# Kernel tuning notes

Measured on AMD Instinct MI355X. Metric: run time of the kernel, lower is better.

Reference implementation:

```python
import jax, jax.numpy as jnp
import numpy as np

DX = 0.5
N_STEPS = 8


def _bilinear_sample(vf, p):
    """Batched bilinear interpolation of vf at points p, clipping to the image domain.
    vf: (B, 2, H, W). p: (B, 2, H, W) with p[:,0]=x (along W), p[:,1]=y (along H)."""
    B, C, H, W = vf.shape
    x = jnp.clip(p[:, 0], 0.0, W - 1.0)
    y = jnp.clip(p[:, 1], 0.0, H - 1.0)
    x0 = jnp.floor(x)
    y0 = jnp.floor(y)
    x1 = jnp.minimum(x0 + 1.0, W - 1.0)
    y1 = jnp.minimum(y0 + 1.0, H - 1.0)
    wx = (x - x0)[:, None]  # (B,1,H,W)
    wy = (y - y0)[:, None]
    x0i, x1i = x0.astype(jnp.int32), x1.astype(jnp.int32)
    y0i, y1i = y0.astype(jnp.int32), y1.astype(jnp.int32)
    vf_flat = vf.reshape(B, C, H * W)

    def gather(yi, xi):
        idx = (yi * W + xi).reshape(B, 1, H * W)
        return jnp.take_along_axis(vf_flat, idx, axis=2).reshape(B, C, H, W)

    v00 = gather(y0i, x0i)
    v01 = gather(y0i, x1i)
    v10 = gather(y1i, x0i)
    v11 = gather(y1i, x1i)
    return (v00 * (1.0 - wx) * (1.0 - wy) + v01 * wx * (1.0 - wy)
            + v10 * (1.0 - wx) * wy + v11 * wx * wy)


def _init_values(B, H, W, dtype):
    # torch: stack(meshgrid(arange(H), arange(W), indexing='ij')[::-1]) -> channel0=x, channel1=y
    gx, gy = jnp.meshgrid(jnp.arange(W, dtype=dtype), jnp.arange(H, dtype=dtype))  # (H,W)
    return jnp.broadcast_to(jnp.stack([gx, gy], axis=0)[None], (B, 2, H, W))


def _trajectories(vf, dx=DX, n_steps=N_STEPS):
    """Euler IVP integration of every pixel through vf. Returns (n_steps+1, B, 2, H, W)."""
    B, C, H, W = vf.shape
    init = _init_values(B, H, W, vf.dtype)

    def step(p, _):
        p_next = p + dx * _bilinear_sample(vf, p)  # euler step
        return p_next, p_next

    _, traj = jax.lax.scan(step, init, None, length=n_steps)
    return jnp.concatenate([init[None], traj], axis=0)


def setup_inputs() -> dict:
    key = jax.random.key(0)
    k1, k2 = jax.random.split(key)
    B, H, W = 8, 512, 512
    vf_pred = jax.random.normal(k1, (B, 2, H, W), dtype=jnp.float32)
    vf_true = jax.random.normal(k2, (B, 2, H, W), dtype=jnp.float32)
    return {"vf_pred": vf_pred, "vf_true": vf_true}


def reference(vf_pred, vf_true):
    true_traj = _trajectories(vf_true)
    pred_traj = _trajectories(vf_pred)
    return jnp.mean((true_traj - pred_traj) ** 2)
```

## Files before the change

kernel.cpp:

```cpp
#include <hip/hip_runtime.h>
#include <hip/hip_fp16.h>

#define HH 512
#define WW 512
#define BB 8
#define HW (HH * WW)
#define DXS 0.5f
#define NSTEPS 8

#define R_BLK 4
#define BAND 15
#define LSW 520

typedef float f2  __attribute__((ext_vector_type(2)));
typedef float f4a __attribute__((ext_vector_type(4)));
typedef unsigned int u4a __attribute__((ext_vector_type(4)));

__device__ __forceinline__ f2 h2f(unsigned int h) {
    __half2 v = __builtin_bit_cast(__half2, h);
    float2 f = __half22float2(v);
    return (f2){f.x, f.y};
}
__device__ __forceinline__ unsigned int f2h(float a, float b) {
    __half2 h = __floats2half2_rn(a, b);
    return __builtin_bit_cast(unsigned int, h);
}

__device__ __forceinline__ f2 bilin_lds(const unsigned int* __restrict__ lds,
                                        int band_lo,
                                        const float* __restrict__ g0,
                                        const float* __restrict__ g1,
                                        float px, float py) {
    float x = fminf(fmaxf(px, 0.0f), (float)(WW - 1));
    float y = fminf(fmaxf(py, 0.0f), (float)(HH - 1));
    float x0f = fminf(floorf(x), (float)(WW - 2));
    float y0f = fminf(floorf(y), (float)(HH - 2));
    float wx = x - x0f;
    float wy = y - y0f;
    int xi = (int)x0f;
    int yi = (int)y0f;
    int r = yi - band_lo;
    f2 out;
    if (r >= 0 && r <= BAND - 2) {
        int idx = r * LSW + xi;
        unsigned int a0 = lds[idx];
        unsigned int a1 = lds[idx + 1];
        unsigned int b0 = lds[idx + LSW];
        unsigned int b1 = lds[idx + LSW + 1];
        f2 v00 = h2f(a0), v01 = h2f(a1), v10 = h2f(b0), v11 = h2f(b1);
        f2 top = v00 + wx * (v01 - v00);
        f2 bot = v10 + wx * (v11 - v10);
        out = top + wy * (bot - top);
    } else {
        int i00 = yi * WW + xi;
        float w00 = (1.0f - wx) * (1.0f - wy);
        float w01 = wx * (1.0f - wy);
        float w10 = (1.0f - wx) * wy;
        float w11 = wx * wy;
        out.x = g0[i00] * w00 + g0[i00 + 1] * w01 + g0[i00 + WW] * w10 + g0[i00 + WW + 1] * w11;
        out.y = g1[i00] * w00 + g1[i00 + 1] * w01 + g1[i00 + WW] * w10 + g1[i00 + WW + 1] * w11;
    }
    return out;
}

__global__ __launch_bounds__(256) void ivp_loss_lds(const float* __restrict__ vf_pred,
                                                    const float* __restrict__ vf_true,
                                                    double* __restrict__ acc) {
    __shared__ unsigned int lt[BAND * LSW];
    __shared__ unsigned int lp[BAND * LSW];
    __shared__ float wsum[4];

    int b    = blockIdx.x & 7;
    int rb   = blockIdx.x >> 3;
    int base = rb * R_BLK;
    int band_lo = min(max(base - 5, 0), HH - BAND);

    const float* tg0 = vf_true + (size_t)b * 2 * HW;
    const float* tg1 = tg0 + HW;
    const float* pg0 = vf_pred + (size_t)b * 2 * HW;
    const float* pg1 = pg0 + HW;

    for (int i = threadIdx.x; i < BAND * 128; i += 256) {
        int rl = i >> 7;
        int g  = i & 127;
        int off = (band_lo + rl) * WW + g * 4;
        f4a tx = *(const f4a*)(tg0 + off);
        f4a ty = *(const f4a*)(tg1 + off);
        f4a px = *(const f4a*)(pg0 + off);
        f4a py = *(const f4a*)(pg1 + off);
        u4a wt = { f2h(tx.x, ty.x), f2h(tx.y, ty.y), f2h(tx.z, ty.z), f2h(tx.w, ty.w) };
        u4a wp = { f2h(px.x, py.x), f2h(px.y, py.y), f2h(px.z, py.z), f2h(px.w, py.w) };
        *(u4a*)&lt[rl * LSW + g * 4] = wt;
        *(u4a*)&lp[rl * LSW + g * 4] = wp;
    }
    __syncthreads();

    int lane = threadIdx.x & 63;
    int wv   = threadIdx.x >> 6;
    int row  = base + wv;
    float fy = (float)row;

    float ptx[8], pty[8], ppx[8], ppy[8];
    float sum = 0.0f;

    #pragma unroll
    for (int c = 0; c < 8; ++c) {
        int x  = lane + 64 * c;
        int li = (row - band_lo) * LSW + x;
        f2 vt = h2f(lt[li]);
        f2 vp = h2f(lp[li]);
        float fx = (float)x;
        ptx[c] = fmaf(DXS, vt.x, fx);  pty[c] = fmaf(DXS, vt.y, fy);
        ppx[c] = fmaf(DXS, vp.x, fx);  ppy[c] = fmaf(DXS, vp.y, fy);
        float dx = ptx[c] - ppx[c], dy = pty[c] - ppy[c];
        sum += dx * dx + dy * dy;
    }

    #pragma unroll 1
    for (int s = 1; s < NSTEPS; ++s) {
        #pragma unroll
        for (int c = 0; c < 8; ++c) {
            f2 vt = bilin_lds(lt, band_lo, tg0, tg1, ptx[c], pty[c]);
            f2 vp = bilin_lds(lp, band_lo, pg0, pg1, ppx[c], ppy[c]);
            ptx[c] += DXS * vt.x;  pty[c] += DXS * vt.y;
            ppx[c] += DXS * vp.x;  ppy[c] += DXS * vp.y;
            float dx = ptx[c] - ppx[c], dy = pty[c] - ppy[c];
            sum += dx * dx + dy * dy;
        }
    }

    for (int off = 32; off > 0; off >>= 1)
        sum += __shfl_down(sum, off, 64);
    if (lane == 0) wsum[wv] = sum;
    __syncthreads();
    if (threadIdx.x == 0) {
        double blocksum = (double)wsum[0] + (double)wsum[1]
                        + (double)wsum[2] + (double)wsum[3];
        atomicAdd(acc, blocksum);
    }
}

__global__ void ivp_finalize_kernel(const double* __restrict__ acc,
                                    float* __restrict__ out) {
    const double total = (double)(NSTEPS + 1) * BB * 2 * HW;
    out[0] = (float)(acc[0] / total);
}

extern "C" void kernel_launch(void* const* d_in, const int* in_sizes, int n_in,
                              void* d_out, int out_size, void* d_ws, size_t ws_size,
                              hipStream_t stream) {
    const float* vf_pred = (const float*)d_in[0];
    const float* vf_true = (const float*)d_in[1];
    float* out = (float*)d_out;
    double* acc = (double*)d_ws;

    hipMemsetAsync(d_ws, 0, 16, stream);

    int blocks = BB * (HH / R_BLK);
    ivp_loss_lds<<<blocks, 256, 0, stream>>>(vf_pred, vf_true, acc);
    ivp_finalize_kernel<<<1, 1, 0, stream>>>(acc, out);
}
```

Before: 56.00 us.

## Fuse finalize into main kernel, use half2 bilinear math, shrink LDS stride

Removes the separate finalize kernel launch by having the last block, found through an atomic counter, compute the mean. The LDS bilinear path now interpolates in packed half2 FMA instead of converting each corner to float. The LDS row stride drops from 520 to 512 so the index can be a shift, at the risk of more bank conflicts. Doing the interpolation in half precision adds rounding error to the trajectories.

```diff
diff --git a/kernel.cpp b/kernel.cpp
--- a/kernel.cpp
+++ b/kernel.cpp
@@ -10,7 +10,7 @@
 
 #define R_BLK 4
 #define BAND 15
-#define LSW 520
+#define LSW 512
 
 typedef float f2  __attribute__((ext_vector_type(2)));
 typedef float f4a __attribute__((ext_vector_type(4)));
@@ -41,16 +41,19 @@
     int yi = (int)y0f;
     int r = yi - band_lo;
     f2 out;
-    if (r >= 0 && r <= BAND - 2) {
-        int idx = r * LSW + xi;
-        unsigned int a0 = lds[idx];
-        unsigned int a1 = lds[idx + 1];
-        unsigned int b0 = lds[idx + LSW];
-        unsigned int b1 = lds[idx + LSW + 1];
-        f2 v00 = h2f(a0), v01 = h2f(a1), v10 = h2f(b0), v11 = h2f(b1);
-        f2 top = v00 + wx * (v01 - v00);
-        f2 bot = v10 + wx * (v11 - v10);
-        out = top + wy * (bot - top);
+    if ((unsigned)r <= (unsigned)(BAND - 2)) {
+        int idx = (r << 9) + xi;
+        __half2 v00 = __builtin_bit_cast(__half2, lds[idx]);
+        __half2 v01 = __builtin_bit_cast(__half2, lds[idx + 1]);
+        __half2 v10 = __builtin_bit_cast(__half2, lds[idx + LSW]);
+        __half2 v11 = __builtin_bit_cast(__half2, lds[idx + LSW + 1]);
+        __half2 wxh = __float2half2_rn(wx);
+        __half2 wyh = __float2half2_rn(wy);
+        __half2 top = __hfma2(wxh, __hsub2(v01, v00), v00);
+        __half2 bot = __hfma2(wxh, __hsub2(v11, v10), v10);
+        __half2 o   = __hfma2(wyh, __hsub2(bot, top), top);
+        float2 f = __half22float2(o);
+        out = (f2){f.x, f.y};
     } else {
         int i00 = yi * WW + xi;
         float w00 = (1.0f - wx) * (1.0f - wy);
@@ -65,7 +68,10 @@
 
 __global__ __launch_bounds__(256) void ivp_loss_lds(const float* __restrict__ vf_pred,
                                                     const float* __restrict__ vf_true,
-                                                    double* __restrict__ acc) {
+                                                    double* __restrict__ acc,
+                                                    unsigned int* __restrict__ cnt,
+                                                    float* __restrict__ out,
+                                                    int nblocks) {
     __shared__ unsigned int lt[BAND * LSW];
     __shared__ unsigned int lp[BAND * LSW];
     __shared__ float wsum[4];
@@ -137,13 +143,14 @@
         double blocksum = (double)wsum[0] + (double)wsum[1]
                         + (double)wsum[2] + (double)wsum[3];
         atomicAdd(acc, blocksum);
+        __threadfence();
+        unsigned int done = atomicAdd(cnt, 1u);
+        if (done == (unsigned)(nblocks - 1)) {
+            double total = atomicAdd(acc, 0.0);
+            const double n = (double)(NSTEPS + 1) * BB * 2 * HW;
+            out[0] = (float)(total / n);
+        }
     }
-}
-
-__global__ void ivp_finalize_kernel(const double* __restrict__ acc,
-                                    float* __restrict__ out) {
-    const double total = (double)(NSTEPS + 1) * BB * 2 * HW;
-    out[0] = (float)(acc[0] / total);
 }
 
 extern "C" void kernel_launch(void* const* d_in, const int* in_sizes, int n_in,
@@ -153,10 +160,10 @@
     const float* vf_true = (const float*)d_in[1];
     float* out = (float*)d_out;
     double* acc = (double*)d_ws;
+    unsigned int* cnt = (unsigned int*)((char*)d_ws + 8);
 
     hipMemsetAsync(d_ws, 0, 16, stream);
 
     int blocks = BB * (HH / R_BLK);
-    ivp_loss_lds<<<blocks, 256, 0, stream>>>(vf_pred, vf_true, acc);
-    ivp_finalize_kernel<<<1, 1, 0, stream>>>(acc, out);
+    ivp_loss_lds<<<blocks, 256, 0, stream>>>(vf_pred, vf_true, acc, cnt, out, blocks);
 }
```

Result: slower. 65.13 us (+16.3%).
